# Performance work log

Hardware: AMD Instinct MI355X
Metric: run time of the kernel (lower is better)

The kernel has to match this reference:

```python
import jax, jax.numpy as jnp
import numpy as np

C = 16
STRIDES = (8, 16, 32, 64, 128)
LVL_HW = ((256, 256), (128, 128), (64, 64), (32, 32), (16, 16))
K_POS = 256
K_HN = 2048
IOU_THRESH = 0.6
EPS = 1e-8


def _cross(a, b):
    return a[..., 0] * b[..., 1] - a[..., 1] * b[..., 0]


def _grid_points():
    # MlvlPointGenerator with offset=0.5: (x+0.5)*stride, row-major (y outer)
    pts, scl = [], []
    for lvl, ((h, w), s) in enumerate(zip(LVL_HW, STRIDES)):
        xs = (jnp.arange(w, dtype=jnp.float32) + 0.5) * s
        ys = (jnp.arange(h, dtype=jnp.float32) + 0.5) * s
        yy, xx = jnp.meshgrid(ys, xs, indexing='ij')
        pts.append(jnp.stack([xx.reshape(-1), yy.reshape(-1)], -1))
        scl.append(jnp.full((h * w,), float(lvl), dtype=jnp.float32))
    return jnp.concatenate(pts, 0), jnp.concatenate(scl, 0)


def _convert(cls_l, box_l, ang_l, ctr_l):
    B = cls_l[0].shape[0]
    cls = jnp.concatenate([x.transpose(0, 2, 3, 1).reshape(B, -1, C) for x in cls_l], 1).reshape(-1, C)
    box = jnp.concatenate([jnp.concatenate([b, a], 1).transpose(0, 2, 3, 1).reshape(B, -1, 5)
                           for b, a in zip(box_l, ang_l)], 1).reshape(-1, 5)
    ctr = jnp.concatenate([x.transpose(0, 2, 3, 1).reshape(B, -1, 1) for x in ctr_l], 1).reshape(-1, 1)
    return cls, box, ctr


def _decode(points, pred):  # DistanceAnglePointCoder.decode, angle_version='le90'
    l, t, r, b, a = [pred[..., i] for i in range(5)]
    ca, sa = jnp.cos(a), jnp.sin(a)
    w, h = l + r, t + b
    oxl, oyl = (r - l) * 0.5, (b - t) * 0.5
    ox = ca * oxl - sa * oyl
    oy = sa * oxl + ca * oyl
    an = (a + jnp.pi / 2) % jnp.pi - jnp.pi / 2
    return jnp.stack([points[..., 0] + ox, points[..., 1] + oy, w, h, an], -1)


def _encode(points, gt):  # DistanceAnglePointCoder.encode
    cx, cy, w, h, a = [gt[..., i] for i in range(5)]
    ca, sa = jnp.cos(a), jnp.sin(a)
    dx, dy = points[..., 0] - cx, points[..., 1] - cy
    ox = ca * dx + sa * dy
    oy = -sa * dx + ca * dy
    return jnp.stack([w / 2 + ox, h / 2 + oy, w / 2 - ox, h / 2 - oy, a], -1)


def _inside_mask(points, boxes):  # [M,2],[P,5] -> [M,P]
    cx, cy, w, h, a = [boxes[:, i][None, :] for i in range(5)]
    ca, sa = jnp.cos(a), jnp.sin(a)
    dx = points[:, 0:1] - cx
    dy = points[:, 1:2] - cy
    ox = ca * dx + sa * dy
    oy = -sa * dx + ca * dy
    m = jnp.minimum(jnp.minimum(w / 2 + ox, w / 2 - ox), jnp.minimum(h / 2 + oy, h / 2 - oy))
    return m > 0


def _corners(boxes):  # [N,5] -> [N,4,2]
    cx, cy, w, h, a = [boxes[:, i:i + 1] for i in range(5)]
    ca, sa = jnp.cos(a), jnp.sin(a)
    dx = jnp.array([-0.5, 0.5, 0.5, -0.5], jnp.float32) * w
    dy = jnp.array([-0.5, -0.5, 0.5, 0.5], jnp.float32) * h
    return jnp.stack([cx + dx * ca - dy * sa, cy + dx * sa + dy * ca], -1)


def _inter_area(ca, cb):  # intersection area of two convex quads [4,2],[4,2]
    pa, pb = ca, cb
    da = jnp.roll(ca, -1, 0) - ca
    db = jnp.roll(cb, -1, 0) - cb
    diff = pb[None, :] - pa[:, None]                     # [4,4,2]
    den = _cross(da[:, None], db[None, :])               # [4,4]
    dsafe = jnp.where(jnp.abs(den) < 1e-10, 1.0, den)
    t = _cross(diff, db[None, :]) / dsafe
    u = _cross(diff, da[:, None]) / dsafe
    ok = (jnp.abs(den) > 1e-10) & (t >= 0) & (t <= 1) & (u >= 0) & (u <= 1)
    ipts = pa[:, None] + t[..., None] * da[:, None]

    def inside(p, c):
        e = jnp.roll(c, -1, 0) - c
        s = _cross(e[None, :], p[:, None] - c[None, :])  # [4 pts, 4 edges]
        return jnp.all(s >= -1e-9, 1) | jnp.all(s <= 1e-9, 1)

    pts = jnp.concatenate([ipts.reshape(16, 2), ca, cb], 0)   # [24,2]
    val = jnp.concatenate([ok.reshape(16), inside(ca, cb), inside(cb, ca)], 0)
    n = val.sum()
    ctr = (pts * val[:, None]).sum(0) / jnp.maximum(n, 1)
    pts = jnp.where(val[:, None], pts, ctr)  # invalid pts collapse to centroid (zero area)
    order = jnp.argsort(jnp.arctan2(pts[:, 1] - ctr[1], pts[:, 0] - ctr[0]))
    pts = pts[order]
    area = 0.5 * jnp.abs(jnp.sum(_cross(pts - ctr, jnp.roll(pts, -1, 0) - ctr)))
    return jnp.where(n >= 3, area, 0.0)


def _rotated_iou(b1, b2):  # box_iou_rotated: [M,5],[P,5] -> [M,P]
    c1, c2 = _corners(b1), _corners(b2)
    inter = jax.vmap(lambda x: jax.vmap(lambda y: _inter_area(x, y))(c2))(c1)
    a1 = jnp.abs(b1[:, 2] * b1[:, 3])
    a2 = jnp.abs(b2[:, 2] * b2[:, 3])
    return inter / (a1[:, None] + a2[None, :] - inter + EPS)


def _bce(p, t):
    p = jnp.clip(p, 1e-12, 1.0 - 1e-12)
    return -(t * jnp.log(p) + (1.0 - t) * jnp.log1p(-p))


def _smooth_l1(x, y):  # nn.SmoothL1Loss(reduction='none'), beta=1
    d = jnp.abs(x - y)
    return jnp.where(d < 1.0, 0.5 * d * d, d - 0.5)


def _arsl_loss(t_cls, t_box, t_iou, s_cls, s_box, s_iou):
    # --- teacher targets (torch.no_grad) ---
    t_cls = jax.lax.stop_gradient(t_cls)
    t_box = jax.lax.stop_gradient(t_box)
    t_iou = jax.lax.stop_gradient(t_iou)
    points, scales = _grid_points()
    N = t_cls.shape[0]
    joint = jax.nn.sigmoid(t_cls) * jax.nn.sigmoid(t_iou)   # [N,C]
    max_vals = joint.max(-1)
    class_ind = joint.argmax(-1)
    cand = max_vals >= 0.1
    n_cand = cand.sum()
    mean = jnp.sum(max_vals * cand) / jnp.maximum(n_cand, 1)
    var = jnp.sum(cand * (max_vals - mean) ** 2) / jnp.maximum(n_cand - 1, 1)  # unbiased std
    pos_thresh = jnp.minimum(mean + jnp.sqrt(var), 0.4)
    pos_thresh = jnp.where(n_cand > 0, pos_thresh, jnp.inf)
    pos_mask = max_vals >= pos_thresh
    hn_mask = cand & (max_vals < pos_thresh)
    # fallback: top-10 positives when thresholding yields none
    fb = jnp.zeros((N,), bool).at[jax.lax.top_k(max_vals, 10)[1]].set(True)
    pos_mask = jnp.where(pos_mask.any(), pos_mask, fb)

    sig_t_cls = jax.nn.sigmoid(t_cls)
    sig_t_iou = jax.nn.sigmoid(t_iou[:, 0])
    cls_targets = jnp.where((pos_mask | hn_mask)[:, None], sig_t_cls, 0.0)
    loc_targets = jnp.where(pos_mask[:, None], t_box, 0.0)
    iou_targets = jnp.where(pos_mask, sig_t_iou, 0.0)
    loc_mask = pos_mask.astype(jnp.float32)

    # --- hard negative mining (fixed-capacity top-k selection) ---
    pv, pidx = jax.lax.top_k(jnp.where(pos_mask, max_vals, -1.0), K_POS)
    p_valid = jnp.take(pos_mask, pidx)
    _, hidx = jax.lax.top_k(jnp.where(hn_mask, max_vals, -1.0), K_HN)
    h_valid = jnp.take(hn_mask, hidx)
    pos_bbox = _decode(points[pidx], t_box[pidx])
    hn_pts = points[hidx]
    hn_bbox = _decode(hn_pts, t_box[hidx])
    iou = _rotated_iou(hn_bbox, pos_bbox)                    # [K_HN, K_POS]
    scale_flag = jnp.abs(scales[pidx][None, :] - scales[hidx][:, None]) <= 1.0
    class_flag = class_ind[pidx][None, :] == class_ind[hidx][:, None]
    inside_flag = _inside_mask(hn_pts, pos_bbox)
    valid = (iou >= IOU_THRESH) & class_flag & inside_flag & scale_flag & h_valid[:, None] & p_valid[None, :]
    iou_m = jnp.where(valid, iou, 0.0)
    potential = iou_m.max(-1) > 0.0                          # [K_HN]
    w = jnp.where(valid, pv[None, :], 0.0)                   # pos joint-confidence weights
    agg_bbox = (w[..., None] * pos_bbox[None]).sum(1) / jnp.maximum(w.sum(1), EPS)[:, None]
    agg_ltrba = _encode(hn_pts, agg_bbox)
    loc_targets = loc_targets.at[hidx].set(jnp.where(potential[:, None], agg_ltrba, loc_targets[hidx]))
    loc_mask = loc_mask.at[hidx].set(jnp.where(potential, 1.0, loc_mask[hidx]))

    loc_pos = loc_mask > 0.0
    iou_targets = jnp.where(loc_pos, sig_t_iou, iou_targets)
    cls_t_max = cls_targets.max(-1)
    cls_avg = jnp.sum(cls_t_max * pos_mask)
    loc_w = jnp.where(loc_pos, cls_t_max, 0.0)
    loc_avg = loc_w.sum()
    iou_avg = loc_pos.sum()

    # --- student losses ---
    s_cls_sig = jax.nn.sigmoid(s_cls)
    s_iou_sig = jax.nn.sigmoid(s_iou)
    jc = s_cls_sig * s_iou_sig  # quality focal loss on joint confidence, gamma=2
    loss_cls = jnp.sum(_bce(jc, cls_targets) * jnp.abs(jc - cls_targets) ** 2) / jnp.maximum(cls_avg, EPS)
    loss_iou = jnp.sum(_bce(s_iou_sig[:, 0], iou_targets) * loc_pos) / jnp.maximum(iou_avg, 1)
    loss_box = jnp.sum(_smooth_l1(s_box, loc_targets) * loc_w[:, None]) / jnp.maximum(loc_avg, EPS)
    return jnp.stack([loss_cls, loss_box, loss_iou])


def setup_inputs():
    key = jax.random.key(0)
    ks = jax.random.split(key, 10)
    inp = {}
    k = 0
    for pre in ('t', 's'):
        for i, (h, w) in enumerate(LVL_HW):
            k4 = jax.random.split(ks[k], 4); k += 1
            # sparse teacher/student confidences; positive box distances in image units
            inp[f'{pre}_cls_{i}'] = jax.random.normal(k4[0], (1, C, h, w), jnp.float32) * 3.0 - 12.0
            inp[f'{pre}_box_{i}'] = jax.random.uniform(k4[1], (1, 4, h, w), jnp.float32) * 64.0 + 1.0
            inp[f'{pre}_ang_{i}'] = jax.random.normal(k4[2], (1, 1, h, w), jnp.float32) * 0.5
            inp[f'{pre}_ctr_{i}'] = jax.random.normal(k4[3], (1, 1, h, w), jnp.float32)
    return inp


def reference(t_cls_0, t_cls_1, t_cls_2, t_cls_3, t_cls_4,
              t_box_0, t_box_1, t_box_2, t_box_3, t_box_4,
              t_ang_0, t_ang_1, t_ang_2, t_ang_3, t_ang_4,
              t_ctr_0, t_ctr_1, t_ctr_2, t_ctr_3, t_ctr_4,
              s_cls_0, s_cls_1, s_cls_2, s_cls_3, s_cls_4,
              s_box_0, s_box_1, s_box_2, s_box_3, s_box_4,
              s_ang_0, s_ang_1, s_ang_2, s_ang_3, s_ang_4,
              s_ctr_0, s_ctr_1, s_ctr_2, s_ctr_3, s_ctr_4):
    t = _convert([t_cls_0, t_cls_1, t_cls_2, t_cls_3, t_cls_4],
                 [t_box_0, t_box_1, t_box_2, t_box_3, t_box_4],
                 [t_ang_0, t_ang_1, t_ang_2, t_ang_3, t_ang_4],
                 [t_ctr_0, t_ctr_1, t_ctr_2, t_ctr_3, t_ctr_4])
    s = _convert([s_cls_0, s_cls_1, s_cls_2, s_cls_3, s_cls_4],
                 [s_box_0, s_box_1, s_box_2, s_box_3, s_box_4],
                 [s_ang_0, s_ang_1, s_ang_2, s_ang_3, s_ang_4],
                 [s_ctr_0, s_ctr_1, s_ctr_2, s_ctr_3, s_ctr_4])
    return _arsl_loss(t[0], t[1], t[2], s[0], s[1], s[2])
```

## Files before the change

### kernel.cpp

```cpp
#include <hip/hip_runtime.h>
#include <math.h>

#define NPTS 87296
#define NCLS 16
#define KPOS 256
#define KHN  2048
#define NBLK 341
#define CAP  4096
#define PI_F   3.14159265358979323846f
#define HPI_F  1.57079632679489661923f

struct InPtrs { const float* p[40]; };

__device__ float g_max_vals[NPTS];
__device__ float g_sig_tiou[NPTS];
__device__ float g_sig_cls_max[NPTS];
__device__ int   g_class_ind[NPTS];
__device__ int   g_pos_mask[NPTS];
__device__ int   g_hn_mask[NPTS];
__device__ int   g_hnflag[NPTS];
__device__ float g_loc_targets[NPTS * 5];
__device__ float g_bsum[NBLK];
__device__ float g_bsumsq[NBLK];
__device__ int   g_bcnt[NBLK];
__device__ int   g_bpos[NBLK];
__device__ int   g_bhn[NBLK];
__device__ int   g_total_pos;
__device__ int   g_total_hn;
__device__ int   g_fallback;
__device__ int   g_pos_cand[CAP];
__device__ int   g_hn_cand[CAP];
__device__ int   g_pidx[KPOS];
__device__ int   g_pvalid[KPOS];
__device__ float g_pv[KPOS];
__device__ int   g_hidx[KHN];
__device__ int   g_hvalid[KHN];
__device__ float g_pos_bbox[KPOS * 5];
__device__ float g_pos_cor[KPOS * 8];
__device__ float g_pos_area[KPOS];
__device__ float g_pos_scale[KPOS];
__device__ int   g_pos_class[KPOS];
__device__ float g_hn_px[KHN];
__device__ float g_hn_py[KHN];
__device__ float g_hn_cor[KHN * 8];
__device__ float g_hn_area[KHN];
__device__ float g_hn_scale[KHN];
__device__ int   g_hn_class[KHN];
__device__ float g_partials[NBLK * 6];

__device__ __forceinline__ float sigmoidf(float x) {
  if (x >= 0.f) return 1.f / (1.f + expf(-x));
  float e = expf(x);
  return e / (1.f + e);
}
__device__ __forceinline__ float crs(float ax, float ay, float bx, float by) {
  return ax * by - ay * bx;
}
__device__ __forceinline__ float mod_pos(float x, float y) {
  float r = fmodf(x, y);
  if (r < 0.f) r += y;
  return r;
}
__device__ __forceinline__ void point_info(int n, int& lvl, int& idx, int& hw,
                                           float& px, float& py) {
  int off, wsh; float stride;
  if (n < 65536)      { lvl = 0; off = 0;     wsh = 8; stride = 8.f;   hw = 65536; }
  else if (n < 81920) { lvl = 1; off = 65536; wsh = 7; stride = 16.f;  hw = 16384; }
  else if (n < 86016) { lvl = 2; off = 81920; wsh = 6; stride = 32.f;  hw = 4096; }
  else if (n < 87040) { lvl = 3; off = 86016; wsh = 5; stride = 64.f;  hw = 1024; }
  else                { lvl = 4; off = 87040; wsh = 4; stride = 128.f; hw = 256; }
  idx = n - off;
  int y = idx >> wsh, x = idx & ((1 << wsh) - 1);
  px = ((float)x + 0.5f) * stride;
  py = ((float)y + 0.5f) * stride;
}

__global__ __launch_bounds__(256) void k_prep(InPtrs P) {
  int tid = threadIdx.x;
  int n = blockIdx.x * 256 + tid;
  int lvl, idx, hw; float px, py;
  point_info(n, lvl, idx, hw, px, py);
  const float* cls = P.p[lvl * 4 + 0];
  const float* ctr = P.p[lvl * 4 + 3];
  float stiou = sigmoidf(ctr[idx]);
  float mv = -1.f, scm = 0.f; int ci = 0;
  for (int c = 0; c < NCLS; c++) {
    float sc = sigmoidf(cls[c * hw + idx]);
    if (sc > scm) scm = sc;
    float j = sc * stiou;
    if (j > mv) { mv = j; ci = c; }
  }
  g_max_vals[n] = mv;
  g_class_ind[n] = ci;
  g_sig_tiou[n] = stiou;
  g_sig_cls_max[n] = scm;
  g_hnflag[n] = 0;
  float isc = (mv >= 0.1f) ? 1.f : 0.f;
  __shared__ float r0[256], r1[256], r2[256];
  r0[tid] = isc; r1[tid] = isc * mv; r2[tid] = isc * mv * mv;
  __syncthreads();
  for (int st = 128; st > 0; st >>= 1) {
    if (tid < st) { r0[tid] += r0[tid + st]; r1[tid] += r1[tid + st]; r2[tid] += r2[tid + st]; }
    __syncthreads();
  }
  if (tid == 0) {
    g_bcnt[blockIdx.x] = (int)r0[0];
    g_bsum[blockIdx.x] = r1[0];
    g_bsumsq[blockIdx.x] = r2[0];
  }
}

__global__ __launch_bounds__(256) void k_mask() {
  int tid = threadIdx.x;
  __shared__ float s1[256], s2[256];
  __shared__ int s0[256];
  int c = 0; float s = 0.f, q = 0.f;
  for (int i = tid; i < NBLK; i += 256) { c += g_bcnt[i]; s += g_bsum[i]; q += g_bsumsq[i]; }
  s0[tid] = c; s1[tid] = s; s2[tid] = q; __syncthreads();
  for (int st = 128; st > 0; st >>= 1) {
    if (tid < st) { s0[tid] += s0[tid + st]; s1[tid] += s1[tid + st]; s2[tid] += s2[tid + st]; }
    __syncthreads();
  }
  int nc = s0[0]; float sum = s1[0], sumsq = s2[0];
  float mean = sum / (float)(nc > 1 ? nc : 1);
  float E = sumsq - 2.f * mean * sum + (float)nc * mean * mean;
  if (E < 0.f) E = 0.f;
  float var = E / (float)((nc - 1) > 1 ? (nc - 1) : 1);
  float th = fminf(mean + sqrtf(var), 0.4f);
  if (nc == 0) th = __int_as_float(0x7f800000);

  int n = blockIdx.x * 256 + tid;
  float v = g_max_vals[n];
  int pm = (v >= th) ? 1 : 0;
  int hm = (v >= 0.1f && v < th) ? 1 : 0;
  g_pos_mask[n] = pm; g_hn_mask[n] = hm;
  __syncthreads();
  __shared__ int t0[256], t1[256];
  t0[tid] = pm; t1[tid] = hm; __syncthreads();
  for (int st = 128; st > 0; st >>= 1) {
    if (tid < st) { t0[tid] += t0[tid + st]; t1[tid] += t1[tid + st]; }
    __syncthreads();
  }
  if (tid == 0) { g_bpos[blockIdx.x] = t0[0]; g_bhn[blockIdx.x] = t1[0]; }
}

__global__ __launch_bounds__(256) void k_compact() {
  int tid = threadIdx.x, b = blockIdx.x;
  __shared__ int r0[256], r1[256];
  int cp = 0, ch = 0;
  for (int i = tid; i < NBLK; i += 256) { cp += g_bpos[i]; ch += g_bhn[i]; }
  r0[tid] = cp; r1[tid] = ch; __syncthreads();
  for (int st = 128; st > 0; st >>= 1) {
    if (tid < st) { r0[tid] += r0[tid + st]; r1[tid] += r1[tid + st]; }
    __syncthreads();
  }
  if (b == 0 && tid == 0) {
    g_total_pos = r0[0]; g_total_hn = r1[0];
    g_fallback = (r0[0] == 0) ? 1 : 0;
  }
  __syncthreads();
  cp = 0; ch = 0;
  for (int i = tid; i < b; i += 256) { cp += g_bpos[i]; ch += g_bhn[i]; }
  r0[tid] = cp; r1[tid] = ch; __syncthreads();
  for (int st = 128; st > 0; st >>= 1) {
    if (tid < st) { r0[tid] += r0[tid + st]; r1[tid] += r1[tid + st]; }
    __syncthreads();
  }
  int poff = r0[0], hoff = r1[0];
  __syncthreads();
  int n = b * 256 + tid;
  int pm = g_pos_mask[n], hm = g_hn_mask[n];
  r0[tid] = pm; r1[tid] = hm; __syncthreads();
  for (int off = 1; off < 256; off <<= 1) {
    int ap = (tid >= off) ? r0[tid - off] : 0;
    int ah = (tid >= off) ? r1[tid - off] : 0;
    __syncthreads();
    r0[tid] += ap; r1[tid] += ah;
    __syncthreads();
  }
  if (pm) { int o = poff + r0[tid] - pm; if (o < CAP) g_pos_cand[o] = n; }
  if (hm) { int o = hoff + r1[tid] - hm; if (o < CAP) g_hn_cand[o] = n; }
}

#define MASK_ALL 0
#define MASK_POS 1
#define MASK_HN  2
__device__ __forceinline__ int sel_mask(int mode, int n) {
  return mode == MASK_ALL ? 1 : (mode == MASK_POS ? g_pos_mask[n] : g_hn_mask[n]);
}

__device__ void radix_select_mask(int mode, int K, int* out_idx, int* out_valid, float* out_val,
                                  int* hist, int* scan_a, int* scan_b, int* sh) {
  int tid = threadIdx.x;
  int c = 0;
  for (int n = tid; n < NPTS; n += 1024) if (sel_mask(mode, n)) c++;
  scan_a[tid] = c; __syncthreads();
  for (int st = 512; st > 0; st >>= 1) {
    if (tid < st) scan_a[tid] += scan_a[tid + st];
    __syncthreads();
  }
  int total = scan_a[0];
  __syncthreads();

  unsigned kth = 0u;
  if (total > K) {
    unsigned prefix = 0; int rem = K;
    for (int pass = 0; pass < 4; pass++) {
      int shift = 24 - 8 * pass;
      if (tid < 256) hist[tid] = 0;
      __syncthreads();
      for (int n = tid; n < NPTS; n += 1024) {
        if (sel_mask(mode, n)) {
          unsigned k = __float_as_uint(g_max_vals[n]);
          if (pass == 0 || ((k >> (shift + 8)) == prefix))
            atomicAdd(&hist[(k >> shift) & 255], 1);
        }
      }
      __syncthreads();
      if (tid == 0) {
        int cum = 0, b = 255;
        for (; b > 0; b--) {
          if (cum + hist[b] >= rem) break;
          cum += hist[b];
        }
        sh[0] = (int)((prefix << 8) | (unsigned)b);
        sh[1] = rem - cum;
      }
      __syncthreads();
      prefix = (unsigned)sh[0]; rem = sh[1];
      __syncthreads();
    }
    kth = prefix;
  }

  const int chunk = (NPTS + 1023) / 1024;
  int start = tid * chunk; if (start > NPTS) start = NPTS;
  int end = start + chunk; if (end > NPTS) end = NPTS;
  int cgt = 0, ceq = 0;
  for (int n = start; n < end; n++) {
    if (sel_mask(mode, n)) {
      unsigned k = __float_as_uint(g_max_vals[n]);
      if (k > kth) cgt++;
      else if (k == kth) ceq++;
    }
  }
  scan_a[tid] = cgt; scan_b[tid] = ceq; __syncthreads();
  if (tid == 0) {
    int ag = 0, ae = 0;
    for (int i = 0; i < 1024; i++) {
      int tg = scan_a[i], te = scan_b[i];
      scan_a[i] = ag; scan_b[i] = ae;
      ag += tg; ae += te;
    }
    sh[0] = ag; sh[1] = ae;
  }
  __syncthreads();
  int cnt_gt = sh[0], cnt_eq = sh[1];
  int og = scan_a[tid], oe = cnt_gt + scan_b[tid];
  for (int n = start; n < end; n++) {
    if (sel_mask(mode, n)) {
      unsigned k = __float_as_uint(g_max_vals[n]);
      if (k > kth) {
        out_idx[og] = n; out_valid[og] = 1;
        if (out_val) out_val[og] = g_max_vals[n];
        og++;
      } else if (k == kth) {
        if (oe < K) {
          out_idx[oe] = n; out_valid[oe] = 1;
          if (out_val) out_val[oe] = g_max_vals[n];
        }
        oe++;
      }
    }
  }
  int kmc = K - cnt_gt;
  int used = cnt_gt + (cnt_eq < kmc ? cnt_eq : kmc);
  __syncthreads();
  for (int i = used + tid; i < K; i += 1024) {
    out_idx[i] = 0; out_valid[i] = 0;
    if (out_val) out_val[i] = -1.f;
  }
  __syncthreads();
}

__device__ void radix_select_list(const int* list, int count, int K,
                                  int* out_idx, int* out_valid, float* out_val,
                                  int* hist, int* scan_a, int* scan_b, int* sh) {
  int tid = threadIdx.x;
  unsigned prefix = 0; int rem = K;
  for (int pass = 0; pass < 4; pass++) {
    int shift = 24 - 8 * pass;
    if (tid < 256) hist[tid] = 0;
    __syncthreads();
    for (int i = tid; i < count; i += 1024) {
      unsigned k = __float_as_uint(g_max_vals[list[i]]);
      if (pass == 0 || ((k >> (shift + 8)) == prefix))
        atomicAdd(&hist[(k >> shift) & 255], 1);
    }
    __syncthreads();
    if (tid == 0) {
      int cum = 0, b = 255;
      for (; b > 0; b--) {
        if (cum + hist[b] >= rem) break;
        cum += hist[b];
      }
      sh[0] = (int)((prefix << 8) | (unsigned)b);
      sh[1] = rem - cum;
    }
    __syncthreads();
    prefix = (unsigned)sh[0]; rem = sh[1];
    __syncthreads();
  }
  unsigned kth = prefix;
  int chunk = (count + 1023) / 1024;
  int start = tid * chunk; if (start > count) start = count;
  int end = start + chunk; if (end > count) end = count;
  int cgt = 0, ceq = 0;
  for (int i = start; i < end; i++) {
    unsigned k = __float_as_uint(g_max_vals[list[i]]);
    if (k > kth) cgt++;
    else if (k == kth) ceq++;
  }
  scan_a[tid] = cgt; scan_b[tid] = ceq; __syncthreads();
  if (tid == 0) {
    int ag = 0, ae = 0;
    for (int i = 0; i < 1024; i++) {
      int tg = scan_a[i], te = scan_b[i];
      scan_a[i] = ag; scan_b[i] = ae;
      ag += tg; ae += te;
    }
    sh[0] = ag;
  }
  __syncthreads();
  int cnt_gt = sh[0];
  int og = scan_a[tid], oe = cnt_gt + scan_b[tid];
  for (int i = start; i < end; i++) {
    int n = list[i];
    unsigned k = __float_as_uint(g_max_vals[n]);
    if (k > kth) {
      out_idx[og] = n; out_valid[og] = 1;
      if (out_val) out_val[og] = g_max_vals[n];
      og++;
    } else if (k == kth) {
      if (oe < K) {
        out_idx[oe] = n; out_valid[oe] = 1;
        if (out_val) out_val[oe] = g_max_vals[n];
      }
      oe++;
    }
  }
  __syncthreads();
}

__global__ __launch_bounds__(1024) void k_select() {
  int tid = threadIdx.x;
  __shared__ int hist[256], scan_a[1024], scan_b[1024], sh_i[4];
  int fallback = g_fallback;
  int tp = g_total_pos, thn = g_total_hn;

  if (!fallback && tp <= KPOS) {
    for (int i = tid; i < KPOS; i += 1024) {
      if (i < tp) {
        int n = g_pos_cand[i];
        g_pidx[i] = n; g_pvalid[i] = 1; g_pv[i] = g_max_vals[n];
      } else { g_pidx[i] = 0; g_pvalid[i] = 0; g_pv[i] = -1.f; }
    }
  } else if (!fallback && tp <= CAP) {
    radix_select_list(g_pos_cand, tp, KPOS, g_pidx, g_pvalid, g_pv, hist, scan_a, scan_b, sh_i);
  } else if (!fallback) {
    radix_select_mask(MASK_POS, KPOS, g_pidx, g_pvalid, g_pv, hist, scan_a, scan_b, sh_i);
  } else {
    radix_select_mask(MASK_ALL, 10, g_pidx, g_pvalid, g_pv, hist, scan_a, scan_b, sh_i);
    for (int i = tid; i < 10; i += 1024)
      if (g_pvalid[i]) g_pos_mask[g_pidx[i]] = 1;
    for (int i = 10 + tid; i < KPOS; i += 1024) {
      g_pidx[i] = 0; g_pvalid[i] = 0; g_pv[i] = -1.f;
    }
  }
  __syncthreads();

  if (thn <= KHN) {
    for (int i = tid; i < KHN; i += 1024) {
      if (i < thn) { g_hidx[i] = g_hn_cand[i]; g_hvalid[i] = 1; }
      else { g_hidx[i] = 0; g_hvalid[i] = 0; }
    }
  } else if (thn <= CAP) {
    radix_select_list(g_hn_cand, thn, KHN, g_hidx, g_hvalid, (float*)0, hist, scan_a, scan_b, sh_i);
  } else {
    radix_select_mask(MASK_HN, KHN, g_hidx, g_hvalid, (float*)0, hist, scan_a, scan_b, sh_i);
  }
}

__device__ void decode_box(int n, const InPtrs& P, float* bb, float* cor,
                           float& area, float& scale, int& cls_out,
                           float* opx, float* opy) {
  int lvl, idx, hw; float px, py;
  point_info(n, lvl, idx, hw, px, py);
  const float* box = P.p[lvl * 4 + 1];
  const float* ang = P.p[lvl * 4 + 2];
  float l = box[idx], t = box[hw + idx], r = box[2 * hw + idx], b = box[3 * hw + idx];
  float a = ang[idx];
  float ca = cosf(a), sa = sinf(a);
  float w = l + r, h = t + b;
  float oxl = (r - l) * 0.5f, oyl = (b - t) * 0.5f;
  float ox = ca * oxl - sa * oyl;
  float oy = sa * oxl + ca * oyl;
  float an = mod_pos(a + HPI_F, PI_F) - HPI_F;
  float cx = px + ox, cy = py + oy;
  bb[0] = cx; bb[1] = cy; bb[2] = w; bb[3] = h; bb[4] = an;
  float c2 = cosf(an), s2 = sinf(an);
  const float dxs[4] = {-0.5f, 0.5f, 0.5f, -0.5f};
  const float dys[4] = {-0.5f, -0.5f, 0.5f, 0.5f};
#pragma unroll
  for (int k = 0; k < 4; k++) {
    float dx = dxs[k] * w, dy = dys[k] * h;
    cor[2 * k]     = cx + dx * c2 - dy * s2;
    cor[2 * k + 1] = cy + dx * s2 + dy * c2;
  }
  area = fabsf(w * h);
  scale = (float)lvl;
  cls_out = g_class_ind[n];
  if (opx) { *opx = px; *opy = py; }
}

__global__ __launch_bounds__(256) void k_decode(InPtrs P) {
  int i = blockIdx.x * 256 + threadIdx.x;
  if (i < KPOS) {
    float bb[5] = {0,0,0,0,0}, cor[8] = {0,0,0,0,0,0,0,0};
    float ar = 0.f, sc = 0.f; int cl = 0;
    if (g_pvalid[i]) decode_box(g_pidx[i], P, bb, cor, ar, sc, cl, (float*)0, (float*)0);
#pragma unroll
    for (int k = 0; k < 5; k++) g_pos_bbox[i * 5 + k] = bb[k];
#pragma unroll
    for (int k = 0; k < 8; k++) g_pos_cor[i * 8 + k] = cor[k];
    g_pos_area[i] = ar; g_pos_scale[i] = sc; g_pos_class[i] = cl;
  } else if (i < KPOS + KHN) {
    int h = i - KPOS;
    float bb[5] = {0,0,0,0,0}, cor[8] = {0,0,0,0,0,0,0,0};
    float ar = 0.f, sc = 0.f, px = 0.f, py = 0.f; int cl = 0;
    if (g_hvalid[h]) decode_box(g_hidx[h], P, bb, cor, ar, sc, cl, &px, &py);
#pragma unroll
    for (int k = 0; k < 8; k++) g_hn_cor[h * 8 + k] = cor[k];
    g_hn_area[h] = ar; g_hn_scale[h] = sc; g_hn_class[h] = cl;
    g_hn_px[h] = px; g_hn_py[h] = py;
  }
}

#define BPASS(KK, JJ)                                                      \
  _Pragma("unroll")                                                        \
  for (int i = 0; i < 32; i++) {                                           \
    int l = i ^ (JJ);                                                      \
    if (l > i) {                                                           \
      bool up = ((i & (KK)) == 0);                                         \
      float aa = sa_[i], ab = sa_[l];                                      \
      bool sw = up ? (aa > ab) : (aa < ab);                                \
      sa_[i] = sw ? ab : aa; sa_[l] = sw ? aa : ab;                        \
      float xi = sx_[i], xl = sx_[l];                                      \
      sx_[i] = sw ? xl : xi; sx_[l] = sw ? xi : xl;                        \
      float yi = sy_[i], yl = sy_[l];                                      \
      sy_[i] = sw ? yl : yi; sy_[l] = sw ? yi : yl;                        \
    }                                                                      \
  }

__device__ float inter_area(const float* __restrict__ A, const float* __restrict__ B) {
  float ax[4], ay[4], bx[4], by[4];
#pragma unroll
  for (int i = 0; i < 4; i++) {
    ax[i] = A[2 * i]; ay[i] = A[2 * i + 1];
    bx[i] = B[2 * i]; by[i] = B[2 * i + 1];
  }
  float dax[4], day[4], dbx[4], dby[4];
#pragma unroll
  for (int i = 0; i < 4; i++) {
    int i1 = (i + 1) & 3;
    dax[i] = ax[i1] - ax[i]; day[i] = ay[i1] - ay[i];
    dbx[i] = bx[i1] - bx[i]; dby[i] = by[i1] - by[i];
  }
  float px[24], py[24]; bool val[24];
#pragma unroll
  for (int i = 0; i < 4; i++) {
#pragma unroll
    for (int j = 0; j < 4; j++) {
      float dx = bx[j] - ax[i], dy = by[j] - ay[i];
      float den = crs(dax[i], day[i], dbx[j], dby[j]);
      float ad = fabsf(den);
      float ds = (ad < 1e-10f) ? 1.0f : den;
      float t = crs(dx, dy, dbx[j], dby[j]) / ds;
      float u = crs(dx, dy, dax[i], day[i]) / ds;
      bool ok = (ad > 1e-10f) & (t >= 0.f) & (t <= 1.f) & (u >= 0.f) & (u <= 1.f);
      int k = i * 4 + j;
      px[k] = ax[i] + t * dax[i];
      py[k] = ay[i] + t * day[i];
      val[k] = ok;
    }
  }
#pragma unroll
  for (int i = 0; i < 4; i++) {
    bool ge = true, le = true;
#pragma unroll
    for (int j = 0; j < 4; j++) {
      float s = crs(dbx[j], dby[j], ax[i] - bx[j], ay[i] - by[j]);
      ge = ge && (s >= -1e-9f);
      le = le && (s <= 1e-9f);
    }
    val[16 + i] = ge || le; px[16 + i] = ax[i]; py[16 + i] = ay[i];
  }
#pragma unroll
  for (int j = 0; j < 4; j++) {
    bool ge = true, le = true;
#pragma unroll
    for (int i = 0; i < 4; i++) {
      float s = crs(dax[i], day[i], bx[j] - ax[i], by[j] - ay[i]);
      ge = ge && (s >= -1e-9f);
      le = le && (s <= 1e-9f);
    }
    val[20 + j] = ge || le; px[20 + j] = bx[j]; py[20 + j] = by[j];
  }
  int n = 0; float sx = 0.f, sy = 0.f;
#pragma unroll
  for (int k = 0; k < 24; k++) if (val[k]) { n++; sx += px[k]; sy += py[k]; }
  float dn = (float)(n > 1 ? n : 1);
  float cx = sx / dn, cy = sy / dn;

  float sa_[32], sx_[32], sy_[32];
#pragma unroll
  for (int k = 0; k < 24; k++) {
    float X = val[k] ? px[k] : cx;
    float Y = val[k] ? py[k] : cy;
    sx_[k] = X; sy_[k] = Y;
    sa_[k] = atan2f(Y - cy, X - cx);
  }
#pragma unroll
  for (int k = 24; k < 32; k++) {
    sa_[k] = __int_as_float(0x7f800000);
    sx_[k] = cx; sy_[k] = cy;
  }
  BPASS(2, 1)
  BPASS(4, 2)  BPASS(4, 1)
  BPASS(8, 4)  BPASS(8, 2)  BPASS(8, 1)
  BPASS(16, 8) BPASS(16, 4) BPASS(16, 2) BPASS(16, 1)
  BPASS(32, 16) BPASS(32, 8) BPASS(32, 4) BPASS(32, 2) BPASS(32, 1)

  float s2 = 0.f;
#pragma unroll
  for (int k = 0; k < 24; k++) {
    int k1 = (k + 1) % 24;
    s2 += crs(sx_[k] - cx, sy_[k] - cy, sx_[k1] - cx, sy_[k1] - cy);
  }
  float area = 0.5f * fabsf(s2);
  return (n >= 3) ? area : 0.f;
}

__global__ __launch_bounds__(256) void k_iou() {
  int h = blockIdx.x;
  int j = threadIdx.x;
  if (!g_hvalid[h]) return;
  float wsum = 0.f, wb[5] = {0,0,0,0,0}, anyv = 0.f;
  if (g_pvalid[j]) {
    bool valid = (g_pos_class[j] == g_hn_class[h]) &&
                 (fabsf(g_pos_scale[j] - g_hn_scale[h]) <= 1.0f);
    if (valid) {
      float cx = g_pos_bbox[j * 5 + 0], cy = g_pos_bbox[j * 5 + 1];
      float bw = g_pos_bbox[j * 5 + 2], bh = g_pos_bbox[j * 5 + 3];
      float an = g_pos_bbox[j * 5 + 4];
      float ca = cosf(an), sa = sinf(an);
      float dx = g_hn_px[h] - cx, dy = g_hn_py[h] - cy;
      float ox = ca * dx + sa * dy, oy = -sa * dx + ca * dy;
      float m = fminf(fminf(bw * 0.5f + ox, bw * 0.5f - ox),
                      fminf(bh * 0.5f + oy, bh * 0.5f - oy));
      valid = (m > 0.f);
    }
    if (valid) {
      float inter = inter_area(&g_hn_cor[h * 8], &g_pos_cor[j * 8]);
      float iou = inter / (g_hn_area[h] + g_pos_area[j] - inter + 1e-8f);
      valid = (iou >= 0.6f);
    }
    if (valid) {
      anyv = 1.f;
      float w = g_pv[j];
      wsum = w;
#pragma unroll
      for (int k = 0; k < 5; k++) wb[k] = w * g_pos_bbox[j * 5 + k];
    }
  }
  __shared__ float red[7][256];
  red[0][j] = wsum;
#pragma unroll
  for (int k = 0; k < 5; k++) red[1 + k][j] = wb[k];
  red[6][j] = anyv;
  __syncthreads();
  for (int st = 128; st > 0; st >>= 1) {
    if (j < st)
#pragma unroll
      for (int k = 0; k < 7; k++) red[k][j] += red[k][j + st];
    __syncthreads();
  }
  if (j == 0 && red[6][0] > 0.f) {
    float inv = 1.f / fmaxf(red[0][0], 1e-8f);
    float bb[5];
#pragma unroll
    for (int k = 0; k < 5; k++) bb[k] = red[1 + k][0] * inv;
    float ca = cosf(bb[4]), sa = sinf(bb[4]);
    float dx = g_hn_px[h] - bb[0], dy = g_hn_py[h] - bb[1];
    float ox = ca * dx + sa * dy, oy = -sa * dx + ca * dy;
    int n = g_hidx[h];
    g_loc_targets[n * 5 + 0] = bb[2] * 0.5f + ox;
    g_loc_targets[n * 5 + 1] = bb[3] * 0.5f + oy;
    g_loc_targets[n * 5 + 2] = bb[2] * 0.5f - ox;
    g_loc_targets[n * 5 + 3] = bb[3] * 0.5f - oy;
    g_loc_targets[n * 5 + 4] = bb[4];
    g_hnflag[n] = 1;
  }
}

__global__ __launch_bounds__(256) void k_loss(InPtrs P) {
  int tid = threadIdx.x;
  int n = blockIdx.x * 256 + tid;
  float v0, v1, v2, v3, v4, v5;
  {
    int lvl, idx, hw; float px, py;
    point_info(n, lvl, idx, hw, px, py);
    int pm = g_pos_mask[n], hm = g_hn_mask[n], hf = g_hnflag[n];
    int sel = pm | hm;
    bool lp = (pm | hf) != 0;
    float ctmax = sel ? g_sig_cls_max[n] : 0.f;
    const float* tcls = P.p[lvl * 4 + 0];
    const float* tbox = P.p[lvl * 4 + 1];
    const float* tang = P.p[lvl * 4 + 2];
    const float* scls = P.p[20 + lvl * 4 + 0];
    const float* sbox = P.p[20 + lvl * 4 + 1];
    const float* sang = P.p[20 + lvl * 4 + 2];
    const float* sctr = P.p[20 + lvl * 4 + 3];
    float siou = sigmoidf(sctr[idx]);
    float scl = 0.f;
    for (int c = 0; c < NCLS; c++) {
      float jc = sigmoidf(scls[c * hw + idx]) * siou;
      float ct = sel ? sigmoidf(tcls[c * hw + idx]) : 0.f;
      float p = jc;
      if (p < 1e-12f) p = 1e-12f;
      float pu = 1.f - 1e-12f;
      if (p > pu) p = pu;
      float bce = -(ct * logf(p) + (1.f - ct) * log1pf(-p));
      float d = fabsf(jc - ct);
      scl += bce * d * d;
    }
    v0 = scl;
    float lw = lp ? ctmax : 0.f;
    float tgt[5];
    if (hf) {
#pragma unroll
      for (int k = 0; k < 5; k++) tgt[k] = g_loc_targets[n * 5 + k];
    } else if (pm) {
      tgt[0] = tbox[idx]; tgt[1] = tbox[hw + idx];
      tgt[2] = tbox[2 * hw + idx]; tgt[3] = tbox[3 * hw + idx];
      tgt[4] = tang[idx];
    } else {
#pragma unroll
      for (int k = 0; k < 5; k++) tgt[k] = 0.f;
    }
    float sb = 0.f;
#pragma unroll
    for (int k = 0; k < 5; k++) {
      float sv = (k < 4) ? sbox[k * hw + idx] : sang[idx];
      float d = fabsf(sv - tgt[k]);
      sb += (d < 1.f) ? 0.5f * d * d : d - 0.5f;
    }
    v1 = sb * lw;
    v2 = 0.f;
    if (lp) {
      float p = siou;
      if (p < 1e-12f) p = 1e-12f;
      float pu = 1.f - 1e-12f;
      if (p > pu) p = pu;
      float ti = g_sig_tiou[n];
      v2 = -(ti * logf(p) + (1.f - ti) * log1pf(-p));
    }
    v3 = pm ? ctmax : 0.f;
    v4 = lw;
    v5 = lp ? 1.f : 0.f;
  }
  __shared__ float red[6][256];
  red[0][tid] = v0; red[1][tid] = v1; red[2][tid] = v2;
  red[3][tid] = v3; red[4][tid] = v4; red[5][tid] = v5;
  __syncthreads();
  for (int st = 128; st > 0; st >>= 1) {
    if (tid < st)
#pragma unroll
      for (int k = 0; k < 6; k++) red[k][tid] += red[k][tid + st];
    __syncthreads();
  }
  if (tid == 0)
#pragma unroll
    for (int k = 0; k < 6; k++) g_partials[blockIdx.x * 6 + k] = red[k][0];
}

__global__ __launch_bounds__(256) void k_final(float* out) {
  int tid = threadIdx.x;
  float a[6] = {0,0,0,0,0,0};
  for (int b = tid; b < NBLK; b += 256)
#pragma unroll
    for (int k = 0; k < 6; k++) a[k] += g_partials[b * 6 + k];
  __shared__ float red[6][256];
#pragma unroll
  for (int k = 0; k < 6; k++) red[k][tid] = a[k];
  __syncthreads();
  for (int st = 128; st > 0; st >>= 1) {
    if (tid < st)
#pragma unroll
      for (int k = 0; k < 6; k++) red[k][tid] += red[k][tid + st];
    __syncthreads();
  }
  if (tid == 0) {
    out[0] = red[0][0] / fmaxf(red[3][0], 1e-8f);
    out[1] = red[1][0] / fmaxf(red[4][0], 1e-8f);
    out[2] = red[2][0] / fmaxf(red[5][0], 1.f);
  }
}

extern "C" void kernel_launch(void* const* d_in, const int* in_sizes, int n_in,
                              void* d_out, int out_size, void* d_ws, size_t ws_size,
                              hipStream_t stream) {
  (void)in_sizes; (void)n_in; (void)out_size; (void)d_ws; (void)ws_size;
  InPtrs P;
  for (int i = 0; i < 40; i++) P.p[i] = (const float*)d_in[i];
  k_prep<<<NBLK, 256, 0, stream>>>(P);
  k_mask<<<NBLK, 256, 0, stream>>>();
  k_compact<<<NBLK, 256, 0, stream>>>();
  k_select<<<1, 1024, 0, stream>>>();
  k_decode<<<(KPOS + KHN + 255) / 256, 256, 0, stream>>>(P);
  k_iou<<<KHN, 256, 0, stream>>>();
  k_loss<<<NBLK, 256, 0, stream>>>(P);
  k_final<<<1, 256, 0, stream>>>((float*)d_out);
}
```

Measured before the change: 59.30 us.

## Fuse pipeline into four kernels with last-block reductions and inline box decode

Cuts the pipeline from eight launches to four. The threshold reduction and the final loss reduction now run in whichever block finishes last, detected with atomic counters. Mask and compaction are merged, each block recomputing its prefix offset by rescanning earlier max values, and the single-block select now runs only on an overflow or fallback path. Box decode moves into the IoU kernel, so every block re-decodes all positives, and atan2 in the polygon sort is replaced by a cheaper pseudo-angle. The trade-offs are quadratic rescanning work in compaction, redundant decode, and atomic-counter synchronisation.

```diff
diff --git a/kernel.cpp b/kernel.cpp
--- a/kernel.cpp
+++ b/kernel.cpp
@@ -5,7 +5,7 @@
 #define NCLS 16
 #define KPOS 256
 #define KHN  2048
-#define NBLK 341
+#define TILES 341
 #define CAP  4096
 #define PI_F   3.14159265358979323846f
 #define HPI_F  1.57079632679489661923f
@@ -20,14 +20,11 @@
 __device__ int   g_hn_mask[NPTS];
 __device__ int   g_hnflag[NPTS];
 __device__ float g_loc_targets[NPTS * 5];
-__device__ float g_bsum[NBLK];
-__device__ float g_bsumsq[NBLK];
-__device__ int   g_bcnt[NBLK];
-__device__ int   g_bpos[NBLK];
-__device__ int   g_bhn[NBLK];
-__device__ int   g_total_pos;
-__device__ int   g_total_hn;
-__device__ int   g_fallback;
+__device__ float g_bsum[TILES];
+__device__ float g_bsumsq[TILES];
+__device__ int   g_bcnt[TILES];
+__device__ float g_thresh;
+__device__ int   g_tp, g_thn, g_slow;
 __device__ int   g_pos_cand[CAP];
 __device__ int   g_hn_cand[CAP];
 __device__ int   g_pidx[KPOS];
@@ -35,18 +32,10 @@
 __device__ float g_pv[KPOS];
 __device__ int   g_hidx[KHN];
 __device__ int   g_hvalid[KHN];
-__device__ float g_pos_bbox[KPOS * 5];
-__device__ float g_pos_cor[KPOS * 8];
-__device__ float g_pos_area[KPOS];
-__device__ float g_pos_scale[KPOS];
-__device__ int   g_pos_class[KPOS];
-__device__ float g_hn_px[KHN];
-__device__ float g_hn_py[KHN];
-__device__ float g_hn_cor[KHN * 8];
-__device__ float g_hn_area[KHN];
-__device__ float g_hn_scale[KHN];
-__device__ int   g_hn_class[KHN];
-__device__ float g_partials[NBLK * 6];
+__device__ float g_partials[TILES * 6];
+__device__ unsigned long long g_done_prep = 0ull;
+__device__ unsigned long long g_done_cmp  = 0ull;
+__device__ unsigned long long g_done_loss = 0ull;
 
 __device__ __forceinline__ float sigmoidf(float x) {
   if (x >= 0.f) return 1.f / (1.f + expf(-x));
@@ -60,6 +49,11 @@
   float r = fmodf(x, y);
   if (r < 0.f) r += y;
   return r;
+}
+__device__ __forceinline__ float pseudo_ang(float dx, float dy) {
+  float den = fabsf(dx) + fabsf(dy);
+  if (den == 0.f) return 0.f;
+  return copysignf(1.f - dx / den, dy);
 }
 __device__ __forceinline__ void point_info(int n, int& lvl, int& idx, int& hw,
                                            float& px, float& py) {
@@ -75,113 +69,6 @@
   py = ((float)y + 0.5f) * stride;
 }
 
-__global__ __launch_bounds__(256) void k_prep(InPtrs P) {
-  int tid = threadIdx.x;
-  int n = blockIdx.x * 256 + tid;
-  int lvl, idx, hw; float px, py;
-  point_info(n, lvl, idx, hw, px, py);
-  const float* cls = P.p[lvl * 4 + 0];
-  const float* ctr = P.p[lvl * 4 + 3];
-  float stiou = sigmoidf(ctr[idx]);
-  float mv = -1.f, scm = 0.f; int ci = 0;
-  for (int c = 0; c < NCLS; c++) {
-    float sc = sigmoidf(cls[c * hw + idx]);
-    if (sc > scm) scm = sc;
-    float j = sc * stiou;
-    if (j > mv) { mv = j; ci = c; }
-  }
-  g_max_vals[n] = mv;
-  g_class_ind[n] = ci;
-  g_sig_tiou[n] = stiou;
-  g_sig_cls_max[n] = scm;
-  g_hnflag[n] = 0;
-  float isc = (mv >= 0.1f) ? 1.f : 0.f;
-  __shared__ float r0[256], r1[256], r2[256];
-  r0[tid] = isc; r1[tid] = isc * mv; r2[tid] = isc * mv * mv;
-  __syncthreads();
-  for (int st = 128; st > 0; st >>= 1) {
-    if (tid < st) { r0[tid] += r0[tid + st]; r1[tid] += r1[tid + st]; r2[tid] += r2[tid + st]; }
-    __syncthreads();
-  }
-  if (tid == 0) {
-    g_bcnt[blockIdx.x] = (int)r0[0];
-    g_bsum[blockIdx.x] = r1[0];
-    g_bsumsq[blockIdx.x] = r2[0];
-  }
-}
-
-__global__ __launch_bounds__(256) void k_mask() {
-  int tid = threadIdx.x;
-  __shared__ float s1[256], s2[256];
-  __shared__ int s0[256];
-  int c = 0; float s = 0.f, q = 0.f;
-  for (int i = tid; i < NBLK; i += 256) { c += g_bcnt[i]; s += g_bsum[i]; q += g_bsumsq[i]; }
-  s0[tid] = c; s1[tid] = s; s2[tid] = q; __syncthreads();
-  for (int st = 128; st > 0; st >>= 1) {
-    if (tid < st) { s0[tid] += s0[tid + st]; s1[tid] += s1[tid + st]; s2[tid] += s2[tid + st]; }
-    __syncthreads();
-  }
-  int nc = s0[0]; float sum = s1[0], sumsq = s2[0];
-  float mean = sum / (float)(nc > 1 ? nc : 1);
-  float E = sumsq - 2.f * mean * sum + (float)nc * mean * mean;
-  if (E < 0.f) E = 0.f;
-  float var = E / (float)((nc - 1) > 1 ? (nc - 1) : 1);
-  float th = fminf(mean + sqrtf(var), 0.4f);
-  if (nc == 0) th = __int_as_float(0x7f800000);
-
-  int n = blockIdx.x * 256 + tid;
-  float v = g_max_vals[n];
-  int pm = (v >= th) ? 1 : 0;
-  int hm = (v >= 0.1f && v < th) ? 1 : 0;
-  g_pos_mask[n] = pm; g_hn_mask[n] = hm;
-  __syncthreads();
-  __shared__ int t0[256], t1[256];
-  t0[tid] = pm; t1[tid] = hm; __syncthreads();
-  for (int st = 128; st > 0; st >>= 1) {
-    if (tid < st) { t0[tid] += t0[tid + st]; t1[tid] += t1[tid + st]; }
-    __syncthreads();
-  }
-  if (tid == 0) { g_bpos[blockIdx.x] = t0[0]; g_bhn[blockIdx.x] = t1[0]; }
-}
-
-__global__ __launch_bounds__(256) void k_compact() {
-  int tid = threadIdx.x, b = blockIdx.x;
-  __shared__ int r0[256], r1[256];
-  int cp = 0, ch = 0;
-  for (int i = tid; i < NBLK; i += 256) { cp += g_bpos[i]; ch += g_bhn[i]; }
-  r0[tid] = cp; r1[tid] = ch; __syncthreads();
-  for (int st = 128; st > 0; st >>= 1) {
-    if (tid < st) { r0[tid] += r0[tid + st]; r1[tid] += r1[tid + st]; }
-    __syncthreads();
-  }
-  if (b == 0 && tid == 0) {
-    g_total_pos = r0[0]; g_total_hn = r1[0];
-    g_fallback = (r0[0] == 0) ? 1 : 0;
-  }
-  __syncthreads();
-  cp = 0; ch = 0;
-  for (int i = tid; i < b; i += 256) { cp += g_bpos[i]; ch += g_bhn[i]; }
-  r0[tid] = cp; r1[tid] = ch; __syncthreads();
-  for (int st = 128; st > 0; st >>= 1) {
-    if (tid < st) { r0[tid] += r0[tid + st]; r1[tid] += r1[tid + st]; }
-    __syncthreads();
-  }
-  int poff = r0[0], hoff = r1[0];
-  __syncthreads();
-  int n = b * 256 + tid;
-  int pm = g_pos_mask[n], hm = g_hn_mask[n];
-  r0[tid] = pm; r1[tid] = hm; __syncthreads();
-  for (int off = 1; off < 256; off <<= 1) {
-    int ap = (tid >= off) ? r0[tid - off] : 0;
-    int ah = (tid >= off) ? r1[tid - off] : 0;
-    __syncthreads();
-    r0[tid] += ap; r1[tid] += ah;
-    __syncthreads();
-  }
-  if (pm) { int o = poff + r0[tid] - pm; if (o < CAP) g_pos_cand[o] = n; }
-  if (hm) { int o = hoff + r1[tid] - hm; if (o < CAP) g_hn_cand[o] = n; }
-}
-
 #define MASK_ALL 0
 #define MASK_POS 1
 #define MASK_HN  2
@@ -193,9 +80,9 @@
                                   int* hist, int* scan_a, int* scan_b, int* sh) {
   int tid = threadIdx.x;
   int c = 0;
-  for (int n = tid; n < NPTS; n += 1024) if (sel_mask(mode, n)) c++;
+  for (int n = tid; n < NPTS; n += 256) if (sel_mask(mode, n)) c++;
   scan_a[tid] = c; __syncthreads();
-  for (int st = 512; st > 0; st >>= 1) {
+  for (int st = 128; st > 0; st >>= 1) {
     if (tid < st) scan_a[tid] += scan_a[tid + st];
     __syncthreads();
   }
@@ -207,9 +94,9 @@
     unsigned prefix = 0; int rem = K;
     for (int pass = 0; pass < 4; pass++) {
       int shift = 24 - 8 * pass;
-      if (tid < 256) hist[tid] = 0;
+      hist[tid] = 0;
       __syncthreads();
-      for (int n = tid; n < NPTS; n += 1024) {
+      for (int n = tid; n < NPTS; n += 256) {
         if (sel_mask(mode, n)) {
           unsigned k = __float_as_uint(g_max_vals[n]);
           if (pass == 0 || ((k >> (shift + 8)) == prefix))
@@ -233,7 +120,7 @@
     kth = prefix;
   }
 
-  const int chunk = (NPTS + 1023) / 1024;
+  const int chunk = (NPTS + 255) / 256;
   int start = tid * chunk; if (start > NPTS) start = NPTS;
   int end = start + chunk; if (end > NPTS) end = NPTS;
   int cgt = 0, ceq = 0;
@@ -247,7 +134,7 @@
   scan_a[tid] = cgt; scan_b[tid] = ceq; __syncthreads();
   if (tid == 0) {
     int ag = 0, ae = 0;
-    for (int i = 0; i < 1024; i++) {
+    for (int i = 0; i < 256; i++) {
       int tg = scan_a[i], te = scan_b[i];
       scan_a[i] = ag; scan_b[i] = ae;
       ag += tg; ae += te;
@@ -276,7 +163,7 @@
   int kmc = K - cnt_gt;
   int used = cnt_gt + (cnt_eq < kmc ? cnt_eq : kmc);
   __syncthreads();
-  for (int i = used + tid; i < K; i += 1024) {
+  for (int i = used + tid; i < K; i += 256) {
     out_idx[i] = 0; out_valid[i] = 0;
     if (out_val) out_val[i] = -1.f;
   }
@@ -290,9 +177,9 @@
   unsigned prefix = 0; int rem = K;
   for (int pass = 0; pass < 4; pass++) {
     int shift = 24 - 8 * pass;
-    if (tid < 256) hist[tid] = 0;
-    __syncthreads();
-    for (int i = tid; i < count; i += 1024) {
+    hist[tid] = 0;
+    __syncthreads();
+    for (int i = tid; i < count; i += 256) {
       unsigned k = __float_as_uint(g_max_vals[list[i]]);
       if (pass == 0 || ((k >> (shift + 8)) == prefix))
         atomicAdd(&hist[(k >> shift) & 255], 1);
@@ -312,7 +199,7 @@
     __syncthreads();
   }
   unsigned kth = prefix;
-  int chunk = (count + 1023) / 1024;
+  int chunk = (count + 255) / 256;
   int start = tid * chunk; if (start > count) start = count;
   int end = start + chunk; if (end > count) end = count;
   int cgt = 0, ceq = 0;
@@ -324,7 +211,7 @@
   scan_a[tid] = cgt; scan_b[tid] = ceq; __syncthreads();
   if (tid == 0) {
     int ag = 0, ae = 0;
-    for (int i = 0; i < 1024; i++) {
+    for (int i = 0; i < 256; i++) {
       int tg = scan_a[i], te = scan_b[i];
       scan_a[i] = ag; scan_b[i] = ae;
       ag += tg; ae += te;
@@ -352,42 +239,39 @@
   __syncthreads();
 }
 
-__global__ __launch_bounds__(1024) void k_select() {
+__device__ void slow_select_block(int tp, int thn, int fallback,
+                                  int* hist, int* si0, int* si1, int* sh_i) {
   int tid = threadIdx.x;
-  __shared__ int hist[256], scan_a[1024], scan_b[1024], sh_i[4];
-  int fallback = g_fallback;
-  int tp = g_total_pos, thn = g_total_hn;
-
   if (!fallback && tp <= KPOS) {
-    for (int i = tid; i < KPOS; i += 1024) {
+    for (int i = tid; i < KPOS; i += 256) {
       if (i < tp) {
-        int n = g_pos_cand[i];
-        g_pidx[i] = n; g_pvalid[i] = 1; g_pv[i] = g_max_vals[n];
+        int m = g_pos_cand[i];
+        g_pidx[i] = m; g_pvalid[i] = 1; g_pv[i] = g_max_vals[m];
       } else { g_pidx[i] = 0; g_pvalid[i] = 0; g_pv[i] = -1.f; }
     }
+    __syncthreads();
   } else if (!fallback && tp <= CAP) {
-    radix_select_list(g_pos_cand, tp, KPOS, g_pidx, g_pvalid, g_pv, hist, scan_a, scan_b, sh_i);
+    radix_select_list(g_pos_cand, tp, KPOS, g_pidx, g_pvalid, g_pv, hist, si0, si1, sh_i);
   } else if (!fallback) {
-    radix_select_mask(MASK_POS, KPOS, g_pidx, g_pvalid, g_pv, hist, scan_a, scan_b, sh_i);
+    radix_select_mask(MASK_POS, KPOS, g_pidx, g_pvalid, g_pv, hist, si0, si1, sh_i);
   } else {
-    radix_select_mask(MASK_ALL, 10, g_pidx, g_pvalid, g_pv, hist, scan_a, scan_b, sh_i);
-    for (int i = tid; i < 10; i += 1024)
+    radix_select_mask(MASK_ALL, 10, g_pidx, g_pvalid, g_pv, hist, si0, si1, sh_i);
+    for (int i = tid; i < 10; i += 256)
       if (g_pvalid[i]) g_pos_mask[g_pidx[i]] = 1;
-    for (int i = 10 + tid; i < KPOS; i += 1024) {
+    for (int i = 10 + tid; i < KPOS; i += 256) {
       g_pidx[i] = 0; g_pvalid[i] = 0; g_pv[i] = -1.f;
     }
-  }
-  __syncthreads();
-
+    __syncthreads();
+  }
   if (thn <= KHN) {
-    for (int i = tid; i < KHN; i += 1024) {
+    for (int i = tid; i < KHN; i += 256) {
       if (i < thn) { g_hidx[i] = g_hn_cand[i]; g_hvalid[i] = 1; }
       else { g_hidx[i] = 0; g_hvalid[i] = 0; }
     }
   } else if (thn <= CAP) {
-    radix_select_list(g_hn_cand, thn, KHN, g_hidx, g_hvalid, (float*)0, hist, scan_a, scan_b, sh_i);
+    radix_select_list(g_hn_cand, thn, KHN, g_hidx, g_hvalid, (float*)0, hist, si0, si1, sh_i);
   } else {
-    radix_select_mask(MASK_HN, KHN, g_hidx, g_hvalid, (float*)0, hist, scan_a, scan_b, sh_i);
+    radix_select_mask(MASK_HN, KHN, g_hidx, g_hvalid, (float*)0, hist, si0, si1, sh_i);
   }
 }
 
@@ -423,29 +307,6 @@
   if (opx) { *opx = px; *opy = py; }
 }
 
-__global__ __launch_bounds__(256) void k_decode(InPtrs P) {
-  int i = blockIdx.x * 256 + threadIdx.x;
-  if (i < KPOS) {
-    float bb[5] = {0,0,0,0,0}, cor[8] = {0,0,0,0,0,0,0,0};
-    float ar = 0.f, sc = 0.f; int cl = 0;
-    if (g_pvalid[i]) decode_box(g_pidx[i], P, bb, cor, ar, sc, cl, (float*)0, (float*)0);
-#pragma unroll
-    for (int k = 0; k < 5; k++) g_pos_bbox[i * 5 + k] = bb[k];
-#pragma unroll
-    for (int k = 0; k < 8; k++) g_pos_cor[i * 8 + k] = cor[k];
-    g_pos_area[i] = ar; g_pos_scale[i] = sc; g_pos_class[i] = cl;
-  } else if (i < KPOS + KHN) {
-    int h = i - KPOS;
-    float bb[5] = {0,0,0,0,0}, cor[8] = {0,0,0,0,0,0,0,0};
-    float ar = 0.f, sc = 0.f, px = 0.f, py = 0.f; int cl = 0;
-    if (g_hvalid[h]) decode_box(g_hidx[h], P, bb, cor, ar, sc, cl, &px, &py);
-#pragma unroll
-    for (int k = 0; k < 8; k++) g_hn_cor[h * 8 + k] = cor[k];
-    g_hn_area[h] = ar; g_hn_scale[h] = sc; g_hn_class[h] = cl;
-    g_hn_px[h] = px; g_hn_py[h] = py;
-  }
-}
-
 #define BPASS(KK, JJ)                                                      \
   _Pragma("unroll")                                                        \
   for (int i = 0; i < 32; i++) {                                           \
@@ -528,7 +389,7 @@
     float X = val[k] ? px[k] : cx;
     float Y = val[k] ? py[k] : cy;
     sx_[k] = X; sy_[k] = Y;
-    sa_[k] = atan2f(Y - cy, X - cx);
+    sa_[k] = pseudo_ang(X - cx, Y - cy);
   }
 #pragma unroll
   for (int k = 24; k < 32; k++) {
@@ -551,36 +412,172 @@
   return (n >= 3) ? area : 0.f;
 }
 
-__global__ __launch_bounds__(256) void k_iou() {
-  int h = blockIdx.x;
-  int j = threadIdx.x;
-  if (!g_hvalid[h]) return;
+__global__ __launch_bounds__(256) void k_prep(InPtrs P) {
+  int tid = threadIdx.x;
+  int t = blockIdx.x;
+  int n = t * 256 + tid;
+  __shared__ float r0[256], r1[256], r2[256];
+  __shared__ int   si0[256];
+  __shared__ int   s_last;
+
+  int lvl, idx, hw; float px, py;
+  point_info(n, lvl, idx, hw, px, py);
+  const float* cls = P.p[lvl * 4 + 0];
+  const float* ctr = P.p[lvl * 4 + 3];
+  float stiou = sigmoidf(ctr[idx]);
+  float mv = -1.f, scm = 0.f; int ci = 0;
+  for (int c = 0; c < NCLS; c++) {
+    float sc = sigmoidf(cls[c * hw + idx]);
+    if (sc > scm) scm = sc;
+    float j = sc * stiou;
+    if (j > mv) { mv = j; ci = c; }
+  }
+  g_max_vals[n] = mv;
+  g_class_ind[n] = ci;
+  g_sig_tiou[n] = stiou;
+  g_sig_cls_max[n] = scm;
+  g_hnflag[n] = 0;
+  float isc = (mv >= 0.1f) ? 1.f : 0.f;
+  r0[tid] = isc; r1[tid] = isc * mv; r2[tid] = isc * mv * mv;
+  __syncthreads();
+  for (int st = 128; st > 0; st >>= 1) {
+    if (tid < st) { r0[tid] += r0[tid + st]; r1[tid] += r1[tid + st]; r2[tid] += r2[tid + st]; }
+    __syncthreads();
+  }
+  if (tid == 0) {
+    g_bcnt[t] = (int)r0[0];
+    g_bsum[t] = r1[0];
+    g_bsumsq[t] = r2[0];
+  }
+  __threadfence();
+  if (tid == 0) {
+    unsigned long long v = atomicAdd(&g_done_prep, 1ull);
+    s_last = ((v % (unsigned long long)TILES) == (unsigned long long)(TILES - 1)) ? 1 : 0;
+  }
+  __syncthreads();
+  if (s_last) {
+    __threadfence();
+    int c = 0; float s = 0.f, q = 0.f;
+    for (int i = tid; i < TILES; i += 256) { c += g_bcnt[i]; s += g_bsum[i]; q += g_bsumsq[i]; }
+    __syncthreads();
+    si0[tid] = c; r0[tid] = s; r1[tid] = q; __syncthreads();
+    for (int st = 128; st > 0; st >>= 1) {
+      if (tid < st) { si0[tid] += si0[tid + st]; r0[tid] += r0[tid + st]; r1[tid] += r1[tid + st]; }
+      __syncthreads();
+    }
+    if (tid == 0) {
+      int nc = si0[0]; float sum = r0[0], sumsq = r1[0];
+      float mean = sum / (float)(nc > 1 ? nc : 1);
+      float E = sumsq - 2.f * mean * sum + (float)nc * mean * mean;
+      if (E < 0.f) E = 0.f;
+      float var = E / (float)((nc - 1) > 1 ? (nc - 1) : 1);
+      float th = fminf(mean + sqrtf(var), 0.4f);
+      if (nc == 0) th = __int_as_float(0x7f800000);
+      g_thresh = th;
+    }
+  }
+}
+
+__global__ __launch_bounds__(256) void k_maskcompact() {
+  int tid = threadIdx.x;
+  int t = blockIdx.x;
+  int n = t * 256 + tid;
+  __shared__ int si0[256], si1[256];
+  __shared__ int hist[256];
+  __shared__ int sh_i[2];
+  __shared__ int s_last;
+
+  float th = g_thresh;
+  float v = g_max_vals[n];
+  int pm = (v >= th) ? 1 : 0;
+  int hm = (v >= 0.1f && v < th) ? 1 : 0;
+  g_pos_mask[n] = pm; g_hn_mask[n] = hm;
+
+  int cp = 0, ch = 0;
+  int lim = t * 256;
+  for (int i = tid; i < lim; i += 256) {
+    float u = g_max_vals[i];
+    cp += (u >= th) ? 1 : 0;
+    ch += (u >= 0.1f && u < th) ? 1 : 0;
+  }
+  si0[tid] = cp; si1[tid] = ch; __syncthreads();
+  for (int st = 128; st > 0; st >>= 1) {
+    if (tid < st) { si0[tid] += si0[tid + st]; si1[tid] += si1[tid + st]; }
+    __syncthreads();
+  }
+  int poff = si0[0], hoff = si1[0];
+  __syncthreads();
+
+  si0[tid] = pm; si1[tid] = hm; __syncthreads();
+  for (int off = 1; off < 256; off <<= 1) {
+    int ap = (tid >= off) ? si0[tid - off] : 0;
+    int ah = (tid >= off) ? si1[tid - off] : 0;
+    __syncthreads();
+    si0[tid] += ap; si1[tid] += ah;
+    __syncthreads();
+  }
+  if (pm) { int o = poff + si0[tid] - pm; if (o < CAP) g_pos_cand[o] = n; }
+  if (hm) { int o = hoff + si1[tid] - hm; if (o < CAP) g_hn_cand[o] = n; }
+  if (t == TILES - 1 && tid == 255) {
+    g_tp = poff + si0[255];
+    g_thn = hoff + si1[255];
+  }
+
+  __threadfence();
+  if (tid == 0) {
+    unsigned long long dv = atomicAdd(&g_done_cmp, 1ull);
+    s_last = ((dv % (unsigned long long)TILES) == (unsigned long long)(TILES - 1)) ? 1 : 0;
+  }
+  __syncthreads();
+  if (s_last) {
+    __threadfence();
+    int tp = g_tp, thn = g_thn;
+    int fallback = (tp == 0) ? 1 : 0;
+    int slow = (fallback || tp > KPOS || thn > KHN) ? 1 : 0;
+    if (tid == 0) g_slow = slow;
+    __syncthreads();
+    if (slow) slow_select_block(tp, thn, fallback, hist, si0, si1, sh_i);
+  }
+}
+
+__global__ __launch_bounds__(256) void k_iou(InPtrs P) {
+  const int h = blockIdx.x;
+  const int j = threadIdx.x;
+  const int slow = g_slow;
+  const int tp = g_tp, thn = g_thn;
+
+  const int hv = slow ? g_hvalid[h] : ((h < thn) ? 1 : 0);
+  if (!hv) return;
+  const int nh = slow ? g_hidx[h] : g_hn_cand[h];
+
+  float hbb[5], hcor[8], har, hsc, hpx, hpy; int hcl;
+  decode_box(nh, P, hbb, hcor, har, hsc, hcl, &hpx, &hpy);
+
   float wsum = 0.f, wb[5] = {0,0,0,0,0}, anyv = 0.f;
-  if (g_pvalid[j]) {
-    bool valid = (g_pos_class[j] == g_hn_class[h]) &&
-                 (fabsf(g_pos_scale[j] - g_hn_scale[h]) <= 1.0f);
+  const int pvld = slow ? g_pvalid[j] : ((j < tp) ? 1 : 0);
+  if (pvld) {
+    int m = slow ? g_pidx[j] : g_pos_cand[j];
+    float pv = slow ? g_pv[j] : g_max_vals[m];
+    float pbb[5], pcor[8], par, psc; int pcl;
+    decode_box(m, P, pbb, pcor, par, psc, pcl, (float*)0, (float*)0);
+    bool valid = (pcl == hcl) && (fabsf(psc - hsc) <= 1.0f);
     if (valid) {
-      float cx = g_pos_bbox[j * 5 + 0], cy = g_pos_bbox[j * 5 + 1];
-      float bw = g_pos_bbox[j * 5 + 2], bh = g_pos_bbox[j * 5 + 3];
-      float an = g_pos_bbox[j * 5 + 4];
-      float ca = cosf(an), sa = sinf(an);
-      float dx = g_hn_px[h] - cx, dy = g_hn_py[h] - cy;
+      float ca = cosf(pbb[4]), sa = sinf(pbb[4]);
+      float dx = hpx - pbb[0], dy = hpy - pbb[1];
       float ox = ca * dx + sa * dy, oy = -sa * dx + ca * dy;
-      float m = fminf(fminf(bw * 0.5f + ox, bw * 0.5f - ox),
-                      fminf(bh * 0.5f + oy, bh * 0.5f - oy));
-      valid = (m > 0.f);
+      float mm = fminf(fminf(pbb[2] * 0.5f + ox, pbb[2] * 0.5f - ox),
+                       fminf(pbb[3] * 0.5f + oy, pbb[3] * 0.5f - oy));
+      valid = (mm > 0.f);
     }
     if (valid) {
-      float inter = inter_area(&g_hn_cor[h * 8], &g_pos_cor[j * 8]);
-      float iou = inter / (g_hn_area[h] + g_pos_area[j] - inter + 1e-8f);
+      float inter = inter_area(hcor, pcor);
+      float iou = inter / (har + par - inter + 1e-8f);
       valid = (iou >= 0.6f);
     }
     if (valid) {
-      anyv = 1.f;
-      float w = g_pv[j];
-      wsum = w;
-#pragma unroll
-      for (int k = 0; k < 5; k++) wb[k] = w * g_pos_bbox[j * 5 + k];
+      anyv = 1.f; wsum = pv;
+#pragma unroll
+      for (int k = 0; k < 5; k++) wb[k] = pv * pbb[k];
     }
   }
   __shared__ float red[7][256];
@@ -601,21 +598,23 @@
 #pragma unroll
     for (int k = 0; k < 5; k++) bb[k] = red[1 + k][0] * inv;
     float ca = cosf(bb[4]), sa = sinf(bb[4]);
-    float dx = g_hn_px[h] - bb[0], dy = g_hn_py[h] - bb[1];
+    float dx = hpx - bb[0], dy = hpy - bb[1];
     float ox = ca * dx + sa * dy, oy = -sa * dx + ca * dy;
-    int n = g_hidx[h];
-    g_loc_targets[n * 5 + 0] = bb[2] * 0.5f + ox;
-    g_loc_targets[n * 5 + 1] = bb[3] * 0.5f + oy;
-    g_loc_targets[n * 5 + 2] = bb[2] * 0.5f - ox;
-    g_loc_targets[n * 5 + 3] = bb[3] * 0.5f - oy;
-    g_loc_targets[n * 5 + 4] = bb[4];
-    g_hnflag[n] = 1;
-  }
-}
-
-__global__ __launch_bounds__(256) void k_loss(InPtrs P) {
+    g_loc_targets[nh * 5 + 0] = bb[2] * 0.5f + ox;
+    g_loc_targets[nh * 5 + 1] = bb[3] * 0.5f + oy;
+    g_loc_targets[nh * 5 + 2] = bb[2] * 0.5f - ox;
+    g_loc_targets[nh * 5 + 3] = bb[3] * 0.5f - oy;
+    g_loc_targets[nh * 5 + 4] = bb[4];
+    g_hnflag[nh] = 1;
+  }
+}
+
+__global__ __launch_bounds__(256) void k_loss(InPtrs P, float* out) {
   int tid = threadIdx.x;
-  int n = blockIdx.x * 256 + tid;
+  int t = blockIdx.x;
+  int n = t * 256 + tid;
+  __shared__ float red[6][256];
+  __shared__ int s_last;
   float v0, v1, v2, v3, v4, v5;
   {
     int lvl, idx, hw; float px, py;
@@ -679,7 +678,6 @@
     v4 = lw;
     v5 = lp ? 1.f : 0.f;
   }
-  __shared__ float red[6][256];
   red[0][tid] = v0; red[1][tid] = v1; red[2][tid] = v2;
   red[3][tid] = v3; red[4][tid] = v4; red[5][tid] = v5;
   __syncthreads();
@@ -691,29 +689,35 @@
   }
   if (tid == 0)
 #pragma unroll
-    for (int k = 0; k < 6; k++) g_partials[blockIdx.x * 6 + k] = red[k][0];
-}
-
-__global__ __launch_bounds__(256) void k_final(float* out) {
-  int tid = threadIdx.x;
-  float a[6] = {0,0,0,0,0,0};
-  for (int b = tid; b < NBLK; b += 256)
-#pragma unroll
-    for (int k = 0; k < 6; k++) a[k] += g_partials[b * 6 + k];
-  __shared__ float red[6][256];
-#pragma unroll
-  for (int k = 0; k < 6; k++) red[k][tid] = a[k];
-  __syncthreads();
-  for (int st = 128; st > 0; st >>= 1) {
-    if (tid < st)
-#pragma unroll
-      for (int k = 0; k < 6; k++) red[k][tid] += red[k][tid + st];
-    __syncthreads();
-  }
+    for (int k = 0; k < 6; k++) g_partials[t * 6 + k] = red[k][0];
+
+  __threadfence();
   if (tid == 0) {
-    out[0] = red[0][0] / fmaxf(red[3][0], 1e-8f);
-    out[1] = red[1][0] / fmaxf(red[4][0], 1e-8f);
-    out[2] = red[2][0] / fmaxf(red[5][0], 1.f);
+    unsigned long long dv = atomicAdd(&g_done_loss, 1ull);
+    s_last = ((dv % (unsigned long long)TILES) == (unsigned long long)(TILES - 1)) ? 1 : 0;
+  }
+  __syncthreads();
+  if (s_last) {
+    __threadfence();
+    float a[6] = {0,0,0,0,0,0};
+    for (int i = tid; i < TILES; i += 256)
+#pragma unroll
+      for (int k = 0; k < 6; k++) a[k] += g_partials[i * 6 + k];
+    __syncthreads();
+#pragma unroll
+    for (int k = 0; k < 6; k++) red[k][tid] = a[k];
+    __syncthreads();
+    for (int st = 128; st > 0; st >>= 1) {
+      if (tid < st)
+#pragma unroll
+        for (int k = 0; k < 6; k++) red[k][tid] += red[k][tid + st];
+      __syncthreads();
+    }
+    if (tid == 0) {
+      out[0] = red[0][0] / fmaxf(red[3][0], 1e-8f);
+      out[1] = red[1][0] / fmaxf(red[4][0], 1e-8f);
+      out[2] = red[2][0] / fmaxf(red[5][0], 1.f);
+    }
   }
 }
 
@@ -723,12 +727,8 @@
   (void)in_sizes; (void)n_in; (void)out_size; (void)d_ws; (void)ws_size;
   InPtrs P;
   for (int i = 0; i < 40; i++) P.p[i] = (const float*)d_in[i];
-  k_prep<<<NBLK, 256, 0, stream>>>(P);
-  k_mask<<<NBLK, 256, 0, stream>>>();
-  k_compact<<<NBLK, 256, 0, stream>>>();
-  k_select<<<1, 1024, 0, stream>>>();
-  k_decode<<<(KPOS + KHN + 255) / 256, 256, 0, stream>>>(P);
-  k_iou<<<KHN, 256, 0, stream>>>();
-  k_loss<<<NBLK, 256, 0, stream>>>(P);
-  k_final<<<1, 256, 0, stream>>>((float*)d_out);
-}
+  k_prep<<<TILES, 256, 0, stream>>>(P);
+  k_maskcompact<<<TILES, 256, 0, stream>>>();
+  k_iou<<<KHN, 256, 0, stream>>>(P);
+  k_loss<<<TILES, 256, 0, stream>>>(P, (float*)d_out);
+}
```

After: 154.9 us. +161.3%, slower.
